# Kernel optimization log

Hardware: AMD Instinct MI355X
Metric: run time of the kernel (lower is better)

Reference implementation:

```python
import jax, jax.numpy as jnp
import numpy as np
from jax import lax

_SIGMA = 1.5
_KSIZE = 5
_THRESH = 30.0
# TF rgb_to_grayscale luma weights
_RGB_W = np.array([0.2989, 0.5870, 0.1140], dtype=np.float32)

def _gauss1d():
    x = np.arange(_KSIZE, dtype=np.float32) - (_KSIZE - 1) / 2.0
    g = np.exp(-(x ** 2) / (2.0 * _SIGMA ** 2))
    return (g / g.sum()).astype(np.float32)

def _conv2d_same(x, k2d):
    # x: [B,H,W,1], k2d: [kh,kw]; reflect padding (TF image-op convention), valid conv
    kh, kw = k2d.shape
    ph, pw = kh // 2, kw // 2
    xp = jnp.pad(x, ((0, 0), (ph, ph), (pw, pw), (0, 0)), mode='reflect')
    k = k2d.reshape(kh, kw, 1, 1)
    return lax.conv_general_dilated(xp, k, window_strides=(1, 1), padding='VALID',
                                    dimension_numbers=('NHWC', 'HWIO', 'NHWC'))

def setup_inputs() -> dict:
    key = jax.random.key(0)
    inputs = jax.random.uniform(key, (32, 512, 512, 3), dtype=jnp.float32)
    return {"inputs": inputs}

def reference(inputs):
    # 1) grayscale
    gray = jnp.einsum('bhwc,c->bhw', inputs, jnp.asarray(_RGB_W))[..., None]  # [B,H,W,1]
    # 2) 5x5 gaussian blur (separable)
    g1 = jnp.asarray(_gauss1d())
    blurred = _conv2d_same(gray, g1[:, None])   # vertical pass [5,1]
    blurred = _conv2d_same(blurred, g1[None, :])  # horizontal pass [1,5]
    # 3) sobel x / y (3x3)
    kx = jnp.asarray(np.array([[-1, 0, 1], [-2, 0, 2], [-1, 0, 1]], dtype=np.float32))
    ky = jnp.asarray(np.array([[-1, -2, -1], [0, 0, 0], [1, 2, 1]], dtype=np.float32))
    sx = _conv2d_same(blurred, kx)
    sy = _conv2d_same(blurred, ky)
    # 4) magnitude + threshold (direction computed then unused in original; skipped)
    magnitude = jnp.sqrt(sx * sx + sy * sy)
    edges = jnp.where(magnitude > _THRESH, 1.0, 0.0).astype(inputs.dtype)
    return edges
```

## Files before the change

### kernel.cpp

```cpp
#include <hip/hip_runtime.h>

#define IMG_H 512
#define IMG_W 512
#define TW 64
#define TH 32
#define GW 72
#define GH 38
#define GS 72
#define TMH 34
#define TMS 72
#define BH 34
#define BS 68

__device__ __forceinline__ int reflect(int i, int n) {
    i = (i < 0) ? -i : i;
    return (i >= n) ? (2 * n - 2 - i) : i;
}
__device__ __forceinline__ float4 ld4s(const float* p) { return *(const float4*)p; }

__global__ __launch_bounds__(256, 6)
void edge_fused_kernel(const float* __restrict__ in, float* __restrict__ out) {
    const int bx0 = blockIdx.x * TW;
    const int by0 = blockIdx.y * TH;
    const int b   = blockIdx.z;
    const int tid = threadIdx.x;

    __shared__ float A[GH * GS];
    __shared__ float Bf[TMH * TMS + 8];

    const float g0 = 0.12007838f, g1 = 0.23388076f, g2 = 0.29208171f;
    const float wr = 0.2989f, wg = 0.5870f, wb = 0.1140f;

    const float* img = in + (size_t)b * (IMG_H * IMG_W * 3);
    const int gx0 = bx0 - 4;

    if (gx0 >= 0 && gx0 + GW <= IMG_W) {
        for (int idx = tid; idx < GH * 18; idx += 256) {
            const int i = idx / 18, g4 = idx % 18;
            const int gy = reflect(by0 - 3 + i, IMG_H);
            const float* rp = img + (size_t)gy * (IMG_W * 3) + (gx0 + 4 * g4) * 3;
            const float4 v0 = ld4s(rp);
            const float4 v1 = ld4s(rp + 4);
            const float4 v2 = ld4s(rp + 8);
            float4 g;
            g.x = v0.x * wr + v0.y * wg + v0.z * wb;
            g.y = v0.w * wr + v1.x * wg + v1.y * wb;
            g.z = v1.z * wr + v1.w * wg + v2.x * wb;
            g.w = v2.y * wr + v2.z * wg + v2.w * wb;
            *(float4*)&A[i * GS + 4 * g4] = g;
        }
    } else {
        for (int idx = tid; idx < GH * GW; idx += 256) {
            const int i = idx / GW, j = idx % GW;
            const int gy = reflect(by0 - 3 + i, IMG_H);
            const int gx = reflect(gx0 + j, IMG_W);
            const float* p = img + (size_t)gy * (IMG_W * 3) + gx * 3;
            A[i * GS + j] = p[0] * wr + p[1] * wg + p[2] * wb;
        }
    }
    __syncthreads();

    for (int idx = tid; idx < TMH * 18; idx += 256) {
        const int i = idx / 18, g4 = idx % 18;
        const float* c = &A[i * GS + 4 * g4];
        const float4 r0 = ld4s(c);
        const float4 r1 = ld4s(c + GS);
        const float4 r2 = ld4s(c + 2 * GS);
        const float4 r3 = ld4s(c + 3 * GS);
        const float4 r4 = ld4s(c + 4 * GS);
        float4 t;
        t.x = g0 * (r0.x + r4.x) + g1 * (r1.x + r3.x) + g2 * r2.x;
        t.y = g0 * (r0.y + r4.y) + g1 * (r1.y + r3.y) + g2 * r2.y;
        t.z = g0 * (r0.z + r4.z) + g1 * (r1.z + r3.z) + g2 * r2.z;
        t.w = g0 * (r0.w + r4.w) + g1 * (r1.w + r3.w) + g2 * r2.w;
        *(float4*)&Bf[i * TMS + 4 * g4] = t;
    }
    __syncthreads();

    for (int idx = tid; idx < BH * 17; idx += 256) {
        const int i = idx / 17, g4 = idx % 17;
        const float* c = &Bf[i * TMS + 4 * g4];
        const float4 a = ld4s(c);
        const float4 d = ld4s(c + 4);
        const float4 e = ld4s(c + 8);
        float4 o;
        o.x = g0 * (a.y + d.y) + g1 * (a.z + d.x) + g2 * a.w;
        o.y = g0 * (a.z + d.z) + g1 * (a.w + d.y) + g2 * d.x;
        o.z = g0 * (a.w + d.w) + g1 * (d.x + d.z) + g2 * d.y;
        o.w = g0 * (d.x + e.x) + g1 * (d.y + d.w) + g2 * d.z;
        *(float4*)&A[i * BS + 4 * g4] = o;
    }
    __syncthreads();

    const int xg = tid & 15;
    const int x  = xg * 4;
    float* ob = out + (size_t)b * (IMG_H * IMG_W) + (size_t)by0 * IMG_W + bx0;
    for (int y = tid >> 4; y < TH; y += 16) {
        const float* r0 = &A[y * BS + x];
        float t[8], m[8], bo[8];
        float4 q;
        q = ld4s(r0);          t[0]=q.x; t[1]=q.y; t[2]=q.z; t[3]=q.w;
        q = ld4s(r0 + 4);      t[4]=q.x; t[5]=q.y; t[6]=q.z; t[7]=q.w;
        q = ld4s(r0 + BS);     m[0]=q.x; m[1]=q.y; m[2]=q.z; m[3]=q.w;
        q = ld4s(r0 + BS + 4); m[4]=q.x; m[5]=q.y; m[6]=q.z; m[7]=q.w;
        q = ld4s(r0 + 2*BS);   bo[0]=q.x; bo[1]=q.y; bo[2]=q.z; bo[3]=q.w;
        q = ld4s(r0 + 2*BS+4); bo[4]=q.x; bo[5]=q.y; bo[6]=q.z; bo[7]=q.w;
        float res[4];
        #pragma unroll
        for (int k = 0; k < 4; ++k) {
            const float tl = t[k],  tc = t[k+1],  tr = t[k+2];
            const float ml = m[k],                 mr = m[k+2];
            const float bl = bo[k], bc = bo[k+1], br = bo[k+2];
            const float sx = (tr - tl) + 2.0f * (mr - ml) + (br - bl);
            const float sy = (bl - tl) + 2.0f * (bc - tc) + (br - tr);
            const float m2 = sx * sx + sy * sy;
            res[k] = (m2 > 900.0f) ? 1.0f : 0.0f;
        }
        float4 rv; rv.x = res[0]; rv.y = res[1]; rv.z = res[2]; rv.w = res[3];
        *(float4*)&ob[(size_t)y * IMG_W + x] = rv;
    }
}

extern "C" void kernel_launch(void* const* d_in, const int* in_sizes, int n_in,
                              void* d_out, int out_size, void* d_ws, size_t ws_size,
                              hipStream_t stream) {
    const float* in = (const float*)d_in[0];
    float* out = (float*)d_out;
    const int B = in_sizes[0] / (IMG_H * IMG_W * 3);
    dim3 grid(IMG_W / TW, IMG_H / TH, B);
    dim3 block(256, 1, 1);
    edge_fused_kernel<<<grid, block, 0, stream>>>(in, out);
}
```

Measured before the change: 161.7 us.

## Store intermediate blur in bf16 shared memory and raise occupancy, batch gray loads

The vertical-blur intermediate buffer is stored as truncated bf16 in shared memory, halving its footprint so launch bounds can go from 6 to 8 blocks per CU. The interior grayscale load is unrolled into three explicit batched vectorized loads to increase memory-level parallelism. Edge tiles now use the vectorized path for most columns and only compute the 4 reflected columns scalar-wise. The bf16 truncation reduces precision of the blurred values and may flip threshold decisions near the edge cutoff.

```diff
diff --git a/kernel.cpp b/kernel.cpp
--- a/kernel.cpp
+++ b/kernel.cpp
@@ -17,94 +17,122 @@
     return (i >= n) ? (2 * n - 2 - i) : i;
 }
 __device__ __forceinline__ float4 ld4s(const float* p) { return *(const float4*)p; }
+__device__ __forceinline__ ushort pkbf(float f) { return (ushort)(__builtin_bit_cast(unsigned, f) >> 16); }
+__device__ __forceinline__ float  upbf(ushort u) { return __builtin_bit_cast(float, (unsigned)u << 16); }
 
-__global__ __launch_bounds__(256, 6)
+#define GRAY4(v0, v1, v2, dst) do { \
+    float4 g_; \
+    g_.x = (v0).x * wr + (v0).y * wg + (v0).z * wb; \
+    g_.y = (v0).w * wr + (v1).x * wg + (v1).y * wb; \
+    g_.z = (v1).z * wr + (v1).w * wg + (v2).x * wb; \
+    g_.w = (v2).y * wr + (v2).z * wg + (v2).w * wb; \
+    *(float4*)(dst) = g_; \
+} while (0)
+
+__global__ __launch_bounds__(256, 8)
 void edge_fused_kernel(const float* __restrict__ in, float* __restrict__ out) {
     const int bx0 = blockIdx.x * TW;
     const int by0 = blockIdx.y * TH;
     const int b   = blockIdx.z;
     const int tid = threadIdx.x;
 
-    __shared__ float A[GH * GS];
-    __shared__ float Bf[TMH * TMS + 8];
+    __shared__ float  A[GH * GS];
+    __shared__ ushort Bf[TMH * TMS + 8];
 
-    const float g0 = 0.12007838f, g1 = 0.23388076f, g2 = 0.29208171f;
+    const float kg0 = 0.12007838f, kg1 = 0.23388076f, kg2 = 0.29208171f;
     const float wr = 0.2989f, wg = 0.5870f, wb = 0.1140f;
 
     const float* img = in + (size_t)b * (IMG_H * IMG_W * 3);
     const int gx0 = bx0 - 4;
+    const bool left  = (bx0 == 0);
+    const bool right = (bx0 + TW == IMG_W);
 
-    if (gx0 >= 0 && gx0 + GW <= IMG_W) {
-        for (int idx = tid; idx < GH * 18; idx += 256) {
-            const int i = idx / 18, g4 = idx % 18;
+    if (!left && !right) {
+        const int idxA = tid, idxB = tid + 256, idxC = tid + 512;
+        const int iA = idxA / 18, jA = idxA % 18;
+        const int iB = idxB / 18, jB = idxB % 18;
+        const int iC = idxC / 18, jC = idxC % 18;
+        const bool hasC = (idxC < GH * 18);
+        const float* rpA = img + (size_t)reflect(by0 - 3 + iA, IMG_H) * (IMG_W * 3) + (gx0 + 4 * jA) * 3;
+        const float* rpB = img + (size_t)reflect(by0 - 3 + iB, IMG_H) * (IMG_W * 3) + (gx0 + 4 * jB) * 3;
+        const float4 a0 = ld4s(rpA), a1 = ld4s(rpA + 4), a2 = ld4s(rpA + 8);
+        const float4 b0 = ld4s(rpB), b1 = ld4s(rpB + 4), b2 = ld4s(rpB + 8);
+        GRAY4(a0, a1, a2, &A[iA * GS + 4 * jA]);
+        float4 c0, c1, c2;
+        if (hasC) {
+            const float* rpC = img + (size_t)reflect(by0 - 3 + iC, IMG_H) * (IMG_W * 3) + (gx0 + 4 * jC) * 3;
+            c0 = ld4s(rpC); c1 = ld4s(rpC + 4); c2 = ld4s(rpC + 8);
+        }
+        GRAY4(b0, b1, b2, &A[iB * GS + 4 * jB]);
+        if (hasC) GRAY4(c0, c1, c2, &A[iC * GS + 4 * jC]);
+    } else {
+        const int go = left ? 1 : 0;
+        for (int idx = tid; idx < GH * 17; idx += 256) {
+            const int i = idx / 17, g = idx % 17 + go;
             const int gy = reflect(by0 - 3 + i, IMG_H);
-            const float* rp = img + (size_t)gy * (IMG_W * 3) + (gx0 + 4 * g4) * 3;
-            const float4 v0 = ld4s(rp);
-            const float4 v1 = ld4s(rp + 4);
-            const float4 v2 = ld4s(rp + 8);
-            float4 g;
-            g.x = v0.x * wr + v0.y * wg + v0.z * wb;
-            g.y = v0.w * wr + v1.x * wg + v1.y * wb;
-            g.z = v1.z * wr + v1.w * wg + v2.x * wb;
-            g.w = v2.y * wr + v2.z * wg + v2.w * wb;
-            *(float4*)&A[i * GS + 4 * g4] = g;
+            const float* rp = img + (size_t)gy * (IMG_W * 3) + (gx0 + 4 * g) * 3;
+            const float4 v0 = ld4s(rp), v1 = ld4s(rp + 4), v2 = ld4s(rp + 8);
+            GRAY4(v0, v1, v2, &A[i * GS + 4 * g]);
         }
-    } else {
-        for (int idx = tid; idx < GH * GW; idx += 256) {
-            const int i = idx / GW, j = idx % GW;
+        const int jbase = left ? 0 : 68;
+        for (int idx = tid; idx < GH * 4; idx += 256) {
+            const int i = idx / 4, j = idx % 4;
             const int gy = reflect(by0 - 3 + i, IMG_H);
-            const int gx = reflect(gx0 + j, IMG_W);
+            const int gx = reflect(gx0 + jbase + j, IMG_W);
             const float* p = img + (size_t)gy * (IMG_W * 3) + gx * 3;
-            A[i * GS + j] = p[0] * wr + p[1] * wg + p[2] * wb;
+            A[i * GS + jbase + j] = p[0] * wr + p[1] * wg + p[2] * wb;
         }
     }
     __syncthreads();
 
     for (int idx = tid; idx < TMH * 18; idx += 256) {
-        const int i = idx / 18, g4 = idx % 18;
-        const float* c = &A[i * GS + 4 * g4];
+        const int i = idx / 18, g = idx % 18;
+        const float* c = &A[i * GS + 4 * g];
         const float4 r0 = ld4s(c);
         const float4 r1 = ld4s(c + GS);
         const float4 r2 = ld4s(c + 2 * GS);
         const float4 r3 = ld4s(c + 3 * GS);
         const float4 r4 = ld4s(c + 4 * GS);
-        float4 t;
-        t.x = g0 * (r0.x + r4.x) + g1 * (r1.x + r3.x) + g2 * r2.x;
-        t.y = g0 * (r0.y + r4.y) + g1 * (r1.y + r3.y) + g2 * r2.y;
-        t.z = g0 * (r0.z + r4.z) + g1 * (r1.z + r3.z) + g2 * r2.z;
-        t.w = g0 * (r0.w + r4.w) + g1 * (r1.w + r3.w) + g2 * r2.w;
-        *(float4*)&Bf[i * TMS + 4 * g4] = t;
+        ushort4 u;
+        u.x = pkbf(kg0 * (r0.x + r4.x) + kg1 * (r1.x + r3.x) + kg2 * r2.x);
+        u.y = pkbf(kg0 * (r0.y + r4.y) + kg1 * (r1.y + r3.y) + kg2 * r2.y);
+        u.z = pkbf(kg0 * (r0.z + r4.z) + kg1 * (r1.z + r3.z) + kg2 * r2.z);
+        u.w = pkbf(kg0 * (r0.w + r4.w) + kg1 * (r1.w + r3.w) + kg2 * r2.w);
+        *(ushort4*)&Bf[i * TMS + 4 * g] = u;
     }
     __syncthreads();
 
     for (int idx = tid; idx < BH * 17; idx += 256) {
-        const int i = idx / 17, g4 = idx % 17;
-        const float* c = &Bf[i * TMS + 4 * g4];
-        const float4 a = ld4s(c);
-        const float4 d = ld4s(c + 4);
-        const float4 e = ld4s(c + 8);
+        const int i = idx / 17, g = idx % 17;
+        const ushort* c = &Bf[i * TMS + 4 * g];
+        const ushort4 ua = *(const ushort4*)c;
+        const ushort4 ub = *(const ushort4*)(c + 4);
+        const float a1 = upbf(ua.y), a2 = upbf(ua.z), a3 = upbf(ua.w);
+        const float d0 = upbf(ub.x), d1 = upbf(ub.y), d2 = upbf(ub.z), d3 = upbf(ub.w);
+        const float e0 = upbf(c[8]);
         float4 o;
-        o.x = g0 * (a.y + d.y) + g1 * (a.z + d.x) + g2 * a.w;
-        o.y = g0 * (a.z + d.z) + g1 * (a.w + d.y) + g2 * d.x;
-        o.z = g0 * (a.w + d.w) + g1 * (d.x + d.z) + g2 * d.y;
-        o.w = g0 * (d.x + e.x) + g1 * (d.y + d.w) + g2 * d.z;
-        *(float4*)&A[i * BS + 4 * g4] = o;
+        o.x = kg0 * (a1 + d1) + kg1 * (a2 + d0) + kg2 * a3;
+        o.y = kg0 * (a2 + d2) + kg1 * (a3 + d1) + kg2 * d0;
+        o.z = kg0 * (a3 + d3) + kg1 * (d0 + d2) + kg2 * d1;
+        o.w = kg0 * (d0 + e0) + kg1 * (d1 + d3) + kg2 * d2;
+        *(float4*)&A[i * BS + 4 * g] = o;
     }
     __syncthreads();
 
-    const int xg = tid & 15;
-    const int x  = xg * 4;
+    const int x = (tid & 15) * 4;
     float* ob = out + (size_t)b * (IMG_H * IMG_W) + (size_t)by0 * IMG_W + bx0;
-    for (int y = tid >> 4; y < TH; y += 16) {
+    #pragma unroll
+    for (int yy = 0; yy < 2; ++yy) {
+        const int y = (tid >> 4) + 16 * yy;
         const float* r0 = &A[y * BS + x];
         float t[8], m[8], bo[8];
         float4 q;
-        q = ld4s(r0);          t[0]=q.x; t[1]=q.y; t[2]=q.z; t[3]=q.w;
-        q = ld4s(r0 + 4);      t[4]=q.x; t[5]=q.y; t[6]=q.z; t[7]=q.w;
-        q = ld4s(r0 + BS);     m[0]=q.x; m[1]=q.y; m[2]=q.z; m[3]=q.w;
-        q = ld4s(r0 + BS + 4); m[4]=q.x; m[5]=q.y; m[6]=q.z; m[7]=q.w;
-        q = ld4s(r0 + 2*BS);   bo[0]=q.x; bo[1]=q.y; bo[2]=q.z; bo[3]=q.w;
-        q = ld4s(r0 + 2*BS+4); bo[4]=q.x; bo[5]=q.y; bo[6]=q.z; bo[7]=q.w;
+        q = ld4s(r0);            t[0]=q.x; t[1]=q.y; t[2]=q.z; t[3]=q.w;
+        q = ld4s(r0 + 4);        t[4]=q.x; t[5]=q.y; t[6]=q.z; t[7]=q.w;
+        q = ld4s(r0 + BS);       m[0]=q.x; m[1]=q.y; m[2]=q.z; m[3]=q.w;
+        q = ld4s(r0 + BS + 4);   m[4]=q.x; m[5]=q.y; m[6]=q.z; m[7]=q.w;
+        q = ld4s(r0 + 2*BS);     bo[0]=q.x; bo[1]=q.y; bo[2]=q.z; bo[3]=q.w;
+        q = ld4s(r0 + 2*BS + 4); bo[4]=q.x; bo[5]=q.y; bo[6]=q.z; bo[7]=q.w;
         float res[4];
         #pragma unroll
         for (int k = 0; k < 4; ++k) {
```

Result: faster. 153.6 us (-5.0%).
